# Kernel tuning notes

Hardware: AMD Instinct MI355X
Metric: run time of the kernel (lower is better)

## Reference

```python
import jax, jax.numpy as jnp
import numpy as np

N, F, H, C = 16384, 512, 16, 16

def setup_inputs() -> dict:
    key = jax.random.key(0)
    ks = jax.random.split(key, 8)
    x = jax.random.normal(ks[0], (N, F), dtype=jnp.float32)
    adjacency = jax.random.uniform(ks[1], (N, N), dtype=jnp.float32)
    W1 = jax.random.normal(ks[2], (F, H), dtype=jnp.float32) * (1.0 / np.sqrt(F))
    b1 = jnp.zeros((H,), dtype=jnp.float32)
    W2 = jax.random.normal(ks[3], (H, C), dtype=jnp.float32) * (1.0 / np.sqrt(H))
    b2 = jnp.zeros((C,), dtype=jnp.float32)
    Wd = jax.random.normal(ks[4], (C, 1), dtype=jnp.float32) * (1.0 / np.sqrt(C))
    bd = jnp.zeros((1,), dtype=jnp.float32)
    return {"x": x, "adjacency": adjacency, "W1": W1, "b1": b1,
            "W2": W2, "b2": b2, "Wd": Wd, "bd": bd}

def reference(x, adjacency, W1, b1, W2, b2, Wd, bd):
    # GCN layer 1: relu(A @ (X @ W1) + b1)   -- [N,F]@[F,16] then [N,N]@[N,16]
    h = jax.nn.relu(adjacency @ (x @ W1) + b1)
    # dropout is a no-op at inference (training=False)
    # GCN layer 2: softmax(A @ (h @ W2) + b2) over classes
    h = jax.nn.softmax(adjacency @ (h @ W2) + b2, axis=-1)
    # dense head: linear activation -> [N, 1]
    out = h @ Wd + bd
    return out
```

## Files before the change

kernel.cpp:

```cpp
#include <hip/hip_runtime.h>
#include <hip/hip_bf16.h>

#define N_NODES 16384
#define FDIM 512

typedef __attribute__((address_space(1))) const void gvoid_t;
typedef __attribute__((address_space(3))) void lvoid_t;
typedef float vfloat4 __attribute__((ext_vector_type(4)));

#define SCHED_FENCE() __builtin_amdgcn_sched_barrier(0)

template <int KTOT, int RELU, int HASBIAS, int FUSE>
__global__ __launch_bounds__(256, 2)
void k_rowagg(const float* __restrict__ A,
              const float* __restrict__ V,
              const float* __restrict__ bias,
              float* __restrict__ out,
              const float* __restrict__ w2,
              const float* __restrict__ wd,
              const float* __restrict__ bdp) {
    constexpr int KT = 256;
    constexpr int NT = KTOT / KT;
    constexpr int TB = KT * 16 * 4;
    __shared__ char lv[2 * TB];

    const int tid = threadIdx.x;
    const int lane = tid & 63;
    const int w = tid >> 6;
    const size_t row0 = (size_t)blockIdx.x * 16 + (size_t)w * 4;

    int sw_src[4];
#pragma unroll
    for (int s = 0; s < 4; ++s) {
        const int D = s * 4096 + tid * 16;
        sw_src[s] = (D ^ (((D >> 8) & 7) << 4)) >> 2;
    }

    unsigned zoff = 0;

    auto STAGE = [&](int halfoff, int t) {
        const float* vt = V + (size_t)t * (KT * 16);
#pragma unroll
        for (int s = 0; s < 4; ++s) {
            __builtin_amdgcn_global_load_lds(
                (gvoid_t*)(const void*)(vt + sw_src[s]),
                (lvoid_t*)(void*)(lv + zoff + halfoff + s * 4096 + tid * 16),
                16, 0, 0);
        }
    };

    auto LOADA = [&](vfloat4 (&a)[4], int t) {
#pragma unroll
        for (int r = 0; r < 4; ++r)
            a[r] = __builtin_nontemporal_load(
                reinterpret_cast<const vfloat4*>(
                    A + (row0 + r) * (size_t)KTOT + (size_t)t * KT + lane * 4));
    };

    float acc[4][16];
#pragma unroll
    for (int r = 0; r < 4; ++r)
#pragma unroll
        for (int c = 0; c < 16; ++c) acc[r][c] = 0.f;

    auto COMPUTE = [&](const vfloat4 (&a)[4], unsigned roff) {
#pragma unroll
        for (int kk = 0; kk < 4; ++kk) {
            vfloat4 vv[4];
#pragma unroll
            for (int cc = 0; cc < 4; ++cc) {
                const unsigned B = (unsigned)lane * 256u + ((unsigned)kk << 6) +
                                   ((unsigned)cc << 4);
                const unsigned P = B ^ (((unsigned)lane & 7u) << 4);
                vv[cc] = *reinterpret_cast<const vfloat4*>(lv + roff + P);
            }
#pragma unroll
            for (int cc = 0; cc < 4; ++cc) {
#pragma unroll
                for (int r = 0; r < 4; ++r) {
                    const float ak = a[r][kk];
                    acc[r][cc * 4 + 0] += ak * vv[cc][0];
                    acc[r][cc * 4 + 1] += ak * vv[cc][1];
                    acc[r][cc * 4 + 2] += ak * vv[cc][2];
                    acc[r][cc * 4 + 3] += ak * vv[cc][3];
                }
            }
        }
    };

    vfloat4 a0[4], a1[4];

    STAGE(0, 0);
    SCHED_FENCE();
    LOADA(a0, 0);
    SCHED_FENCE();
    asm volatile("s_waitcnt vmcnt(4)" ::: "memory");
    __builtin_amdgcn_s_barrier();
    asm volatile("" : "+v"(zoff));
    SCHED_FENCE();

#pragma unroll 1
    for (int t = 0; t < NT; t += 2) {
        STAGE(TB, t + 1);
        SCHED_FENCE();
        LOADA(a1, t + 1);
        SCHED_FENCE();
        COMPUTE(a0, zoff + 0);
        SCHED_FENCE();
        asm volatile("s_waitcnt vmcnt(4)" ::: "memory");
        __builtin_amdgcn_s_barrier();
        asm volatile("" : "+v"(zoff));
        SCHED_FENCE();

        if (t + 2 < NT) {
            STAGE(0, t + 2);
            SCHED_FENCE();
            LOADA(a0, t + 2);
            SCHED_FENCE();
            COMPUTE(a1, zoff + TB);
            SCHED_FENCE();
            asm volatile("s_waitcnt vmcnt(4)" ::: "memory");
            __builtin_amdgcn_s_barrier();
            asm volatile("" : "+v"(zoff));
            SCHED_FENCE();
        } else {
            COMPUTE(a1, zoff + TB);
        }
    }

    float o = 0.f;
#pragma unroll
    for (int r = 0; r < 4; ++r) {
#pragma unroll
        for (int c = 0; c < 16; ++c) {
            float s = acc[r][c];
            s += __shfl_xor(s, 1);  s += __shfl_xor(s, 2);  s += __shfl_xor(s, 4);
            s += __shfl_xor(s, 8);  s += __shfl_xor(s, 16); s += __shfl_xor(s, 32);
            o = (r * 16 + c == lane) ? s : o;
        }
    }
    if (HASBIAS) o += bias[lane & 15];
    if (RELU) o = fmaxf(o, 0.f);

    if (FUSE == 0) {
        out[row0 * 16 + lane] = o;
    } else if (FUSE == 1) {
        const int c = lane & 15;
        float s = 0.f;
#pragma unroll
        for (int k = 0; k < 16; ++k) {
            const float hk = __shfl(o, (lane & 48) + k);
            s += hk * w2[k * 16 + c];
        }
        out[row0 * 16 + lane] = s;
    } else {
        const int c = lane & 15;
        float m = o;
        m = fmaxf(m, __shfl_xor(m, 1));
        m = fmaxf(m, __shfl_xor(m, 2));
        m = fmaxf(m, __shfl_xor(m, 4));
        m = fmaxf(m, __shfl_xor(m, 8));
        const float e = expf(o - m);
        float se = e, sd = e * wd[c];
        se += __shfl_xor(se, 1); sd += __shfl_xor(sd, 1);
        se += __shfl_xor(se, 2); sd += __shfl_xor(sd, 2);
        se += __shfl_xor(se, 4); sd += __shfl_xor(sd, 4);
        se += __shfl_xor(se, 8); sd += __shfl_xor(sd, 8);
        if (c == 0) out[row0 + (lane >> 4)] = sd / se + bdp[0];
    }
}

extern "C" void kernel_launch(void* const* d_in, const int* in_sizes, int n_in,
                              void* d_out, int out_size, void* d_ws, size_t ws_size,
                              hipStream_t stream) {
    const float* x  = (const float*)d_in[0];
    const float* A  = (const float*)d_in[1];
    const float* W1 = (const float*)d_in[2];
    const float* b1 = (const float*)d_in[3];
    const float* W2 = (const float*)d_in[4];
    const float* b2 = (const float*)d_in[5];
    const float* Wd = (const float*)d_in[6];
    const float* bd = (const float*)d_in[7];
    float* out = (float*)d_out;

    float* ws = (float*)d_ws;
    float* xw = ws;
    float* hw = ws + 1 * N_NODES * 16;

    k_rowagg<FDIM, 0, 0, 0><<<N_NODES / 16, 256, 0, stream>>>(
        x, W1, b1, xw, nullptr, nullptr, nullptr);
    k_rowagg<N_NODES, 1, 1, 1><<<N_NODES / 16, 256, 0, stream>>>(
        A, xw, b1, hw, W2, nullptr, nullptr);
    k_rowagg<N_NODES, 0, 1, 2><<<N_NODES / 16, 256, 0, stream>>>(
        A, hw, b2, out, nullptr, Wd, bd);
}
```

Measured before the change: 453.4 us.

## Replace LDS-staged aggregation with direct register loads of V in adjacency kernels

```diff
diff --git a/kernel.cpp b/kernel.cpp
--- a/kernel.cpp
+++ b/kernel.cpp
@@ -10,122 +10,59 @@
 
 #define SCHED_FENCE() __builtin_amdgcn_sched_barrier(0)
 
-template <int KTOT, int RELU, int HASBIAS, int FUSE>
+template <int RELU, int HASBIAS, int FUSE>
 __global__ __launch_bounds__(256, 2)
-void k_rowagg(const float* __restrict__ A,
-              const float* __restrict__ V,
-              const float* __restrict__ bias,
-              float* __restrict__ out,
-              const float* __restrict__ w2,
-              const float* __restrict__ wd,
-              const float* __restrict__ bdp) {
-    constexpr int KT = 256;
-    constexpr int NT = KTOT / KT;
-    constexpr int TB = KT * 16 * 4;
-    __shared__ char lv[2 * TB];
-
+void k_bcast(const float* __restrict__ A,
+             const float* __restrict__ V,
+             const float* __restrict__ bias,
+             float* __restrict__ out,
+             const float* __restrict__ w2,
+             const float* __restrict__ wd,
+             const float* __restrict__ bdp) {
     const int tid = threadIdx.x;
     const int lane = tid & 63;
     const int w = tid >> 6;
     const size_t row0 = (size_t)blockIdx.x * 16 + (size_t)w * 4;
 
-    int sw_src[4];
-#pragma unroll
-    for (int s = 0; s < 4; ++s) {
-        const int D = s * 4096 + tid * 16;
-        sw_src[s] = (D ^ (((D >> 8) & 7) << 4)) >> 2;
-    }
-
-    unsigned zoff = 0;
-
-    auto STAGE = [&](int halfoff, int t) {
-        const float* vt = V + (size_t)t * (KT * 16);
-#pragma unroll
-        for (int s = 0; s < 4; ++s) {
-            __builtin_amdgcn_global_load_lds(
-                (gvoid_t*)(const void*)(vt + sw_src[s]),
-                (lvoid_t*)(void*)(lv + zoff + halfoff + s * 4096 + tid * 16),
-                16, 0, 0);
-        }
-    };
-
-    auto LOADA = [&](vfloat4 (&a)[4], int t) {
+    float acc[4][16];
+#pragma unroll
+    for (int r = 0; r < 4; ++r)
+#pragma unroll
+        for (int c = 0; c < 16; ++c) acc[r][c] = 0.f;
+
+    auto LOADS = [&](int step, float (&a)[4], vfloat4 (&v)[4]) {
+        const size_t kk = (size_t)step * 64 + lane;
 #pragma unroll
         for (int r = 0; r < 4; ++r)
-            a[r] = __builtin_nontemporal_load(
-                reinterpret_cast<const vfloat4*>(
-                    A + (row0 + r) * (size_t)KTOT + (size_t)t * KT + lane * 4));
-    };
-
-    float acc[4][16];
-#pragma unroll
-    for (int r = 0; r < 4; ++r)
-#pragma unroll
-        for (int c = 0; c < 16; ++c) acc[r][c] = 0.f;
-
-    auto COMPUTE = [&](const vfloat4 (&a)[4], unsigned roff) {
-#pragma unroll
-        for (int kk = 0; kk < 4; ++kk) {
-            vfloat4 vv[4];
-#pragma unroll
-            for (int cc = 0; cc < 4; ++cc) {
-                const unsigned B = (unsigned)lane * 256u + ((unsigned)kk << 6) +
-                                   ((unsigned)cc << 4);
-                const unsigned P = B ^ (((unsigned)lane & 7u) << 4);
-                vv[cc] = *reinterpret_cast<const vfloat4*>(lv + roff + P);
+            a[r] = __builtin_nontemporal_load(A + (row0 + r) * (size_t)N_NODES + kk);
+#pragma unroll
+        for (int cc = 0; cc < 4; ++cc)
+            v[cc] = *reinterpret_cast<const vfloat4*>(V + kk * 16 + cc * 4);
+    };
+
+    auto FMAS = [&](const float (&a)[4], const vfloat4 (&v)[4]) {
+#pragma unroll
+        for (int cc = 0; cc < 4; ++cc) {
+#pragma unroll
+            for (int r = 0; r < 4; ++r) {
+                acc[r][cc * 4 + 0] += a[r] * v[cc][0];
+                acc[r][cc * 4 + 1] += a[r] * v[cc][1];
+                acc[r][cc * 4 + 2] += a[r] * v[cc][2];
+                acc[r][cc * 4 + 3] += a[r] * v[cc][3];
             }
-#pragma unroll
-            for (int cc = 0; cc < 4; ++cc) {
-#pragma unroll
-                for (int r = 0; r < 4; ++r) {
-                    const float ak = a[r][kk];
-                    acc[r][cc * 4 + 0] += ak * vv[cc][0];
-                    acc[r][cc * 4 + 1] += ak * vv[cc][1];
-                    acc[r][cc * 4 + 2] += ak * vv[cc][2];
-                    acc[r][cc * 4 + 3] += ak * vv[cc][3];
-                }
-            }
-        }
-    };
-
-    vfloat4 a0[4], a1[4];
-
-    STAGE(0, 0);
-    SCHED_FENCE();
-    LOADA(a0, 0);
-    SCHED_FENCE();
-    asm volatile("s_waitcnt vmcnt(4)" ::: "memory");
-    __builtin_amdgcn_s_barrier();
-    asm volatile("" : "+v"(zoff));
-    SCHED_FENCE();
-
+        }
+    };
+
+    float aX[4], aY[4];
+    vfloat4 vX[4], vY[4];
+
+    LOADS(0, aX, vX);
 #pragma unroll 1
-    for (int t = 0; t < NT; t += 2) {
-        STAGE(TB, t + 1);
-        SCHED_FENCE();
-        LOADA(a1, t + 1);
-        SCHED_FENCE();
-        COMPUTE(a0, zoff + 0);
-        SCHED_FENCE();
-        asm volatile("s_waitcnt vmcnt(4)" ::: "memory");
-        __builtin_amdgcn_s_barrier();
-        asm volatile("" : "+v"(zoff));
-        SCHED_FENCE();
-
-        if (t + 2 < NT) {
-            STAGE(0, t + 2);
-            SCHED_FENCE();
-            LOADA(a0, t + 2);
-            SCHED_FENCE();
-            COMPUTE(a1, zoff + TB);
-            SCHED_FENCE();
-            asm volatile("s_waitcnt vmcnt(4)" ::: "memory");
-            __builtin_amdgcn_s_barrier();
-            asm volatile("" : "+v"(zoff));
-            SCHED_FENCE();
-        } else {
-            COMPUTE(a1, zoff + TB);
-        }
+    for (int s = 0; s < N_NODES / 64; s += 2) {
+        LOADS(s + 1, aY, vY);
+        FMAS(aX, vX);
+        if (s + 2 < N_NODES / 64) LOADS(s + 2, aX, vX);
+        FMAS(aY, vY);
     }
 
     float o = 0.f;
@@ -170,6 +107,137 @@
     }
 }
 
+template <int KTOT, int RELU, int HASBIAS>
+__global__ __launch_bounds__(256, 2)
+void k_rowagg(const float* __restrict__ A,
+              const float* __restrict__ V,
+              const float* __restrict__ bias,
+              float* __restrict__ out) {
+    constexpr int KT = 256;
+    constexpr int NT = KTOT / KT;
+    constexpr int TB = KT * 16 * 4;
+    __shared__ char lv[2 * TB];
+
+    const int tid = threadIdx.x;
+    const int lane = tid & 63;
+    const int w = tid >> 6;
+    const size_t row0 = (size_t)blockIdx.x * 16 + (size_t)w * 4;
+
+    int sw_src[4];
+#pragma unroll
+    for (int s = 0; s < 4; ++s) {
+        const int D = s * 4096 + tid * 16;
+        sw_src[s] = (D ^ (((D >> 8) & 7) << 4)) >> 2;
+    }
+
+    unsigned zoff = 0;
+
+    auto STAGE = [&](int halfoff, int t) {
+        const float* vt = V + (size_t)t * (KT * 16);
+#pragma unroll
+        for (int s = 0; s < 4; ++s) {
+            __builtin_amdgcn_global_load_lds(
+                (gvoid_t*)(const void*)(vt + sw_src[s]),
+                (lvoid_t*)(void*)(lv + zoff + halfoff + s * 4096 + tid * 16),
+                16, 0, 0);
+        }
+    };
+
+    auto LOADA = [&](vfloat4 (&a)[4], int t) {
+#pragma unroll
+        for (int r = 0; r < 4; ++r)
+            a[r] = __builtin_nontemporal_load(
+                reinterpret_cast<const vfloat4*>(
+                    A + (row0 + r) * (size_t)KTOT + (size_t)t * KT + lane * 4));
+    };
+
+    float acc[4][16];
+#pragma unroll
+    for (int r = 0; r < 4; ++r)
+#pragma unroll
+        for (int c = 0; c < 16; ++c) acc[r][c] = 0.f;
+
+    auto COMPUTE = [&](const vfloat4 (&a)[4], unsigned roff) {
+#pragma unroll
+        for (int kk = 0; kk < 4; ++kk) {
+            vfloat4 vv[4];
+#pragma unroll
+            for (int cc = 0; cc < 4; ++cc) {
+                const unsigned B = (unsigned)lane * 256u + ((unsigned)kk << 6) +
+                                   ((unsigned)cc << 4);
+                const unsigned P = B ^ (((unsigned)lane & 7u) << 4);
+                vv[cc] = *reinterpret_cast<const vfloat4*>(lv + roff + P);
+            }
+#pragma unroll
+            for (int cc = 0; cc < 4; ++cc) {
+#pragma unroll
+                for (int r = 0; r < 4; ++r) {
+                    const float ak = a[r][kk];
+                    acc[r][cc * 4 + 0] += ak * vv[cc][0];
+                    acc[r][cc * 4 + 1] += ak * vv[cc][1];
+                    acc[r][cc * 4 + 2] += ak * vv[cc][2];
+                    acc[r][cc * 4 + 3] += ak * vv[cc][3];
+                }
+            }
+        }
+    };
+
+    vfloat4 a0[4], a1[4];
+
+    STAGE(0, 0);
+    SCHED_FENCE();
+    LOADA(a0, 0);
+    SCHED_FENCE();
+    asm volatile("s_waitcnt vmcnt(4)" ::: "memory");
+    __builtin_amdgcn_s_barrier();
+    asm volatile("" : "+v"(zoff));
+    SCHED_FENCE();
+
+#pragma unroll 1
+    for (int t = 0; t < NT; t += 2) {
+        STAGE(TB, t + 1);
+        SCHED_FENCE();
+        LOADA(a1, t + 1);
+        SCHED_FENCE();
+        COMPUTE(a0, zoff + 0);
+        SCHED_FENCE();
+        asm volatile("s_waitcnt vmcnt(4)" ::: "memory");
+        __builtin_amdgcn_s_barrier();
+        asm volatile("" : "+v"(zoff));
+        SCHED_FENCE();
+
+        if (t + 2 < NT) {
+            STAGE(0, t + 2);
+            SCHED_FENCE();
+            LOADA(a0, t + 2);
+            SCHED_FENCE();
+            COMPUTE(a1, zoff + TB);
+            SCHED_FENCE();
+            asm volatile("s_waitcnt vmcnt(4)" ::: "memory");
+            __builtin_amdgcn_s_barrier();
+            asm volatile("" : "+v"(zoff));
+            SCHED_FENCE();
+        } else {
+            COMPUTE(a1, zoff + TB);
+        }
+    }
+
+    float o = 0.f;
+#pragma unroll
+    for (int r = 0; r < 4; ++r) {
+#pragma unroll
+        for (int c = 0; c < 16; ++c) {
+            float s = acc[r][c];
+            s += __shfl_xor(s, 1);  s += __shfl_xor(s, 2);  s += __shfl_xor(s, 4);
+            s += __shfl_xor(s, 8);  s += __shfl_xor(s, 16); s += __shfl_xor(s, 32);
+            o = (r * 16 + c == lane) ? s : o;
+        }
+    }
+    if (HASBIAS) o += bias[lane & 15];
+    if (RELU) o = fmaxf(o, 0.f);
+    out[row0 * 16 + lane] = o;
+}
+
 extern "C" void kernel_launch(void* const* d_in, const int* in_sizes, int n_in,
                               void* d_out, int out_size, void* d_ws, size_t ws_size,
                               hipStream_t stream) {
@@ -187,10 +255,9 @@
     float* xw = ws;
     float* hw = ws + 1 * N_NODES * 16;
 
-    k_rowagg<FDIM, 0, 0, 0><<<N_NODES / 16, 256, 0, stream>>>(
-        x, W1, b1, xw, nullptr, nullptr, nullptr);
-    k_rowagg<N_NODES, 1, 1, 1><<<N_NODES / 16, 256, 0, stream>>>(
+    k_rowagg<FDIM, 0, 0><<<N_NODES / 16, 256, 0, stream>>>(x, W1, b1, xw);
+    k_bcast<1, 1, 1><<<N_NODES / 16, 256, 0, stream>>>(
         A, xw, b1, hw, W2, nullptr, nullptr);
-    k_rowagg<N_NODES, 0, 1, 2><<<N_NODES / 16, 256, 0, stream>>>(
+    k_bcast<0, 1, 2><<<N_NODES / 16, 256, 0, stream>>>(
         A, hw, b2, out, nullptr, Wd, bd);
 }
```

New measurement: 891.6 us. 1.97x slower.
